# Kernel tuning notes

Hardware: AMD Instinct MI355X
Metric: run time of the kernel (lower is better)

The kernel has to match this reference:

```python
import jax, jax.numpy as jnp
import numpy as np


def _gcn_conv(X, src, dst, norm, W, n_nodes):
    # gather + normalized aggregate (SpMM) then dense linear (GEMM)
    msg = X[src] * norm[:, None]                       # [E, F]
    agg = jax.ops.segment_sum(msg, dst, num_segments=n_nodes)  # [N, F]
    return agg @ W                                     # [N, F_out]


def setup_inputs() -> dict:
    key = jax.random.key(0)
    k1, k2, k3, k4, k5 = jax.random.split(key, 5)
    N, E, D_IN, D_HID, D_OUT = 50000, 800000, 128, 128, 64
    X = jax.random.normal(k1, (N, D_IN), dtype=jnp.float32)
    edge_index = jax.random.randint(k2, (2, E), 0, N, dtype=jnp.int64)
    s = 1.0 / np.sqrt(D_IN)
    W1 = jax.random.normal(k3, (D_IN, D_HID), dtype=jnp.float32) * s
    W2 = jax.random.normal(k4, (D_HID, D_HID), dtype=jnp.float32) * s
    W3 = jax.random.normal(k5, (D_HID, D_OUT), dtype=jnp.float32) * s
    return {"X": X, "edge_index": edge_index, "W1": W1, "W2": W2, "W3": W3}


def reference(X, edge_index, W1, W2, W3):
    n_nodes = X.shape[0]
    src, dst = edge_index[0], edge_index[1]
    # symmetric degree normalization D^-1/2 A D^-1/2 (degrees from edge list)
    ones = jnp.ones(src.shape[0], dtype=X.dtype)
    deg = jax.ops.segment_sum(ones, dst, num_segments=n_nodes)
    deg = jnp.maximum(deg, 1.0)
    dinv = jax.lax.rsqrt(deg)
    norm = dinv[src] * dinv[dst]                       # [E]
    h = jax.nn.relu(_gcn_conv(X, src, dst, norm, W1, n_nodes))
    h = jax.nn.relu(_gcn_conv(h, src, dst, norm, W2, n_nodes))
    h = jax.nn.relu(_gcn_conv(h, src, dst, norm, W3, n_nodes))
    return jax.nn.softmax(h, axis=-1)
```

## Files before the change

kernel.cpp:

```cpp
#include <hip/hip_runtime.h>
#include <hip/hip_bf16.h>

typedef __attribute__((ext_vector_type(8))) short short8;
typedef __attribute__((ext_vector_type(4))) short short4v;
typedef __attribute__((ext_vector_type(4))) float f32x4;

static inline size_t ws_align(size_t x) { return (x + 511) & ~((size_t)511); }

static __device__ inline unsigned short f2bf(float f) {
    __hip_bfloat16 h = __float2bfloat16(f);
    return __builtin_bit_cast(unsigned short, h);
}

static __device__ inline float bf2f(unsigned short u) {
    unsigned int x = ((unsigned int)u) << 16;
    return __builtin_bit_cast(float, x);
}

__global__ void sniff_kernel(const unsigned short* __restrict__ w1,
                             const unsigned int* __restrict__ ei,
                             int* __restrict__ flags) {
    int i = threadIdx.x;
    unsigned e = (w1[2 * i] >> 7) & 0xFF;
    unsigned long long m1 = __ballot(e >= 100 && e <= 130);
    unsigned long long m2 = __ballot(ei[2 * i + 1] == 0u);
    if (i == 0) {
        flags[0] = (__popcll(m1) < 48) ? 1 : 0;
        flags[1] = (__popcll(m2) >= 48) ? 1 : 0;
    }
}

__global__ void hist_kernel(const int* __restrict__ ei, const int* __restrict__ flags,
                            int* __restrict__ counts, int* __restrict__ loff, int E) {
    int e = blockIdx.x * blockDim.x + threadIdx.x;
    if (e < E) {
        int d = flags[1] ? ei[2 * (size_t)E + 2 * e] : ei[(size_t)E + e];
        loff[e] = atomicAdd(&counts[d], 1);
    }
}

__global__ __launch_bounds__(256) void alloc_kernel(const int* __restrict__ counts,
                                                    float* __restrict__ dinv,
                                                    int* __restrict__ rowptr,
                                                    int* __restrict__ total, int N) {
    int n = blockIdx.x * blockDim.x + threadIdx.x;
    int lane = threadIdx.x & 63;
    int c = (n < N) ? counts[n] : 0;
    if (n < N) {
        int d = (c < 1) ? 1 : c;
        dinv[n] = rsqrtf((float)d);
    }
    int incl = c;
#pragma unroll
    for (int off = 1; off < 64; off <<= 1) {
        int v = __shfl_up(incl, off, 64);
        if (lane >= off) incl += v;
    }
    int wavetot = __shfl(incl, 63, 64);
    int base = 0;
    if (lane == 0) base = atomicAdd(total, wavetot);
    base = __shfl(base, 0, 64);
    if (n < N) rowptr[n] = base + incl - c;
}

__global__ void fill_kernel(const int* __restrict__ ei, const int* __restrict__ flags,
                            const float* __restrict__ dinv, const int* __restrict__ rowptr,
                            const int* __restrict__ loff, int2* __restrict__ edgedat, int E) {
    int e = blockIdx.x * blockDim.x + threadIdx.x;
    if (e < E) {
        int s, d;
        if (flags[1]) {
            s = ei[2 * e];
            d = ei[2 * (size_t)E + 2 * e];
        } else {
            s = ei[e];
            d = ei[(size_t)E + e];
        }
        int pos = rowptr[d] + loff[e];
        float wt = dinv[s] * dinv[d];
        edgedat[pos] = make_int2(s, __float_as_int(wt));
    }
}


template <int FOUT>
__global__ __launch_bounds__(256) void gemm_kernel(const void* __restrict__ Araw, int a_follows,
                                                   const void* __restrict__ Wraw,
                                                   const int* __restrict__ flags,
                                                   unsigned short* __restrict__ out, int Nrows) {
    constexpr int K = 128;
    constexpr int NT = FOUT / 16;
    constexpr int LDB = K + 8;
    __shared__ __align__(16) unsigned short bt[FOUT * LDB];

    const int tid = threadIdx.x;
    const int in_fp32 = flags[0];
    const int a_fp32 = a_follows & in_fp32;

    constexpr int TOT4 = K * FOUT / 4;
    if (in_fp32) {
        const float* Wf = (const float*)Wraw;
        for (int i = tid; i < TOT4; i += 256) {
            int idx = i * 4;
            int k = idx / FOUT;
            int n = idx & (FOUT - 1);
            float4 v = *(const float4*)(const void*)(Wf + idx);
            bt[(n + 0) * LDB + k] = f2bf(v.x);
            bt[(n + 1) * LDB + k] = f2bf(v.y);
            bt[(n + 2) * LDB + k] = f2bf(v.z);
            bt[(n + 3) * LDB + k] = f2bf(v.w);
        }
    } else {
        const unsigned short* Ws = (const unsigned short*)Wraw;
        for (int i = tid; i < TOT4; i += 256) {
            int idx = i * 4;
            int k = idx / FOUT;
            int n = idx & (FOUT - 1);
            short4v v = *(const short4v*)(const void*)(Ws + idx);
#pragma unroll
            for (int j = 0; j < 4; j++) bt[(n + j) * LDB + k] = ((const unsigned short*)&v)[j];
        }
    }

    const int wave = tid >> 6;
    const int lane = tid & 63;
    const int quad = lane >> 4;
    const int r16 = lane & 15;

    short8 afrag[2][4];
#pragma unroll
    for (int t = 0; t < 2; t++) {
        int arow = blockIdx.x * 128 + t * 64 + wave * 16 + r16;
        if (arow > Nrows - 1) arow = Nrows - 1;
        if (a_fp32) {
            const float* Ap = (const float*)Araw + (size_t)arow * K + quad * 8;
#pragma unroll
            for (int kk = 0; kk < 4; kk++) {
                float4 f0 = *(const float4*)(const void*)(Ap + kk * 32);
                float4 f1 = *(const float4*)(const void*)(Ap + kk * 32 + 4);
                short8 r;
                r[0] = (short)f2bf(f0.x); r[1] = (short)f2bf(f0.y);
                r[2] = (short)f2bf(f0.z); r[3] = (short)f2bf(f0.w);
                r[4] = (short)f2bf(f1.x); r[5] = (short)f2bf(f1.y);
                r[6] = (short)f2bf(f1.z); r[7] = (short)f2bf(f1.w);
                afrag[t][kk] = r;
            }
        } else {
            const unsigned short* Ap = (const unsigned short*)Araw + (size_t)arow * K + quad * 8;
#pragma unroll
            for (int kk = 0; kk < 4; kk++) afrag[t][kk] = *(const short8*)(const void*)(Ap + kk * 32);
        }
    }

    __syncthreads();

    f32x4 acc[2][NT];
#pragma unroll
    for (int t = 0; t < 2; t++)
#pragma unroll
        for (int nt = 0; nt < NT; nt++) acc[t][nt] = (f32x4){0.f, 0.f, 0.f, 0.f};

#pragma unroll
    for (int kk = 0; kk < 4; kk++) {
#pragma unroll
        for (int nt = 0; nt < NT; nt++) {
            short8 b = *(const short8*)(const void*)(&bt[(nt * 16 + r16) * LDB + kk * 32 + quad * 8]);
#pragma unroll
            for (int t = 0; t < 2; t++)
                acc[t][nt] = __builtin_amdgcn_mfma_f32_16x16x32_bf16(afrag[t][kk], b, acc[t][nt], 0, 0, 0);
        }
    }

#pragma unroll
    for (int t = 0; t < 2; t++) {
#pragma unroll
        for (int nt = 0; nt < NT; nt++) {
#pragma unroll
            for (int r = 0; r < 4; r++) {
                float v = acc[t][nt][r];
                float o = __shfl_xor(v, 1, 64);
                int row = blockIdx.x * 128 + t * 64 + wave * 16 + quad * 4 + r;
                if (((lane & 1) == 0) && row < Nrows) {
                    __hip_bfloat162 pk;
                    pk.x = __float2bfloat16(v);
                    pk.y = __float2bfloat16(o);
                    *(__hip_bfloat162*)(out + (size_t)row * FOUT + nt * 16 + r16) = pk;
                }
            }
        }
    }
}


__global__ __launch_bounds__(256) void spmm128_kernel(const int2* __restrict__ edgedat,
                                                      const int* __restrict__ rowptr,
                                                      const int* __restrict__ counts,
                                                      const unsigned short* __restrict__ Hin,
                                                      unsigned short* __restrict__ Hout, int N) {
    int wid = (blockIdx.x * 256 + threadIdx.x) >> 6;
    if (wid >= N) return;
    int lane = threadIdx.x & 63;
    int grp = lane >> 4;
    int gl = lane & 15;
    int n = __builtin_amdgcn_readfirstlane(wid);
    int start = __builtin_amdgcn_readfirstlane(rowptr[n]);
    int len = __builtin_amdgcn_readfirstlane(counts[n]);
    const int2* ep = edgedat + start;

    float acc[8];
#pragma unroll
    for (int u = 0; u < 8; u++) acc[u] = 0.f;

    int j = 0;
    for (; j + 8 <= len; j += 8) {
        int2 e0 = ep[j + grp];
        int2 e1 = ep[j + 4 + grp];
        short8 h0 = *(const short8*)(const void*)(Hin + (size_t)e0.x * 128 + gl * 8);
        short8 h1 = *(const short8*)(const void*)(Hin + (size_t)e1.x * 128 + gl * 8);
        float w0 = __int_as_float(e0.y);
        float w1 = __int_as_float(e1.y);
#pragma unroll
        for (int u = 0; u < 8; u++) acc[u] += w0 * bf2f((unsigned short)h0[u]);
#pragma unroll
        for (int u = 0; u < 8; u++) acc[u] += w1 * bf2f((unsigned short)h1[u]);
    }
    for (; j + 4 <= len; j += 4) {
        int2 e = ep[j + grp];
        short8 h = *(const short8*)(const void*)(Hin + (size_t)e.x * 128 + gl * 8);
        float w = __int_as_float(e.y);
#pragma unroll
        for (int u = 0; u < 8; u++) acc[u] += w * bf2f((unsigned short)h[u]);
    }
    int rem = len - j;
    if (grp < rem) {
        int2 e = ep[j + grp];
        short8 h = *(const short8*)(const void*)(Hin + (size_t)e.x * 128 + gl * 8);
        float w = __int_as_float(e.y);
#pragma unroll
        for (int u = 0; u < 8; u++) acc[u] += w * bf2f((unsigned short)h[u]);
    }

#pragma unroll
    for (int u = 0; u < 8; u++) {
        acc[u] += __shfl_xor(acc[u], 16, 64);
        acc[u] += __shfl_xor(acc[u], 32, 64);
    }

    if (grp == 0) {
        short8 o;
#pragma unroll
        for (int u = 0; u < 8; u++) o[u] = (short)f2bf(fmaxf(acc[u], 0.f));
        *(short8*)(void*)(Hout + (size_t)n * 128 + gl * 8) = o;
    }
}


__global__ __launch_bounds__(256) void spmm64_softmax_kernel(const int2* __restrict__ edgedat,
                                                             const int* __restrict__ rowptr,
                                                             const int* __restrict__ counts,
                                                             const unsigned short* __restrict__ Hin,
                                                             const int* __restrict__ flags,
                                                             void* __restrict__ Out, int N) {
    int wid = (blockIdx.x * 256 + threadIdx.x) >> 6;
    if (wid >= N) return;
    int lane = threadIdx.x & 63;
    int grp = lane >> 3;
    int gl = lane & 7;
    int n = __builtin_amdgcn_readfirstlane(wid);
    int start = __builtin_amdgcn_readfirstlane(rowptr[n]);
    int len = __builtin_amdgcn_readfirstlane(counts[n]);
    const int2* ep = edgedat + start;

    float acc[8];
#pragma unroll
    for (int u = 0; u < 8; u++) acc[u] = 0.f;

    int j = 0;
    for (; j + 16 <= len; j += 16) {
        int2 e0 = ep[j + grp];
        int2 e1 = ep[j + 8 + grp];
        short8 h0 = *(const short8*)(const void*)(Hin + (size_t)e0.x * 64 + gl * 8);
        short8 h1 = *(const short8*)(const void*)(Hin + (size_t)e1.x * 64 + gl * 8);
        float w0 = __int_as_float(e0.y);
        float w1 = __int_as_float(e1.y);
#pragma unroll
        for (int u = 0; u < 8; u++) acc[u] += w0 * bf2f((unsigned short)h0[u]);
#pragma unroll
        for (int u = 0; u < 8; u++) acc[u] += w1 * bf2f((unsigned short)h1[u]);
    }
    for (; j + 8 <= len; j += 8) {
        int2 e = ep[j + grp];
        short8 h = *(const short8*)(const void*)(Hin + (size_t)e.x * 64 + gl * 8);
        float w = __int_as_float(e.y);
#pragma unroll
        for (int u = 0; u < 8; u++) acc[u] += w * bf2f((unsigned short)h[u]);
    }
    int rem = len - j;
    if (grp < rem) {
        int2 e = ep[j + grp];
        short8 h = *(const short8*)(const void*)(Hin + (size_t)e.x * 64 + gl * 8);
        float w = __int_as_float(e.y);
#pragma unroll
        for (int u = 0; u < 8; u++) acc[u] += w * bf2f((unsigned short)h[u]);
    }

#pragma unroll
    for (int u = 0; u < 8; u++) {
        acc[u] += __shfl_xor(acc[u], 8, 64);
        acc[u] += __shfl_xor(acc[u], 16, 64);
        acc[u] += __shfl_xor(acc[u], 32, 64);
    }

#pragma unroll
    for (int u = 0; u < 8; u++) acc[u] = fmaxf(acc[u], 0.f);

    float m = acc[0];
#pragma unroll
    for (int u = 1; u < 8; u++) m = fmaxf(m, acc[u]);
#pragma unroll
    for (int off = 1; off < 8; off <<= 1) m = fmaxf(m, __shfl_xor(m, off, 64));

    float ex[8];
    float s = 0.f;
#pragma unroll
    for (int u = 0; u < 8; u++) {
        ex[u] = __expf(acc[u] - m);
        s += ex[u];
    }
#pragma unroll
    for (int off = 1; off < 8; off <<= 1) s += __shfl_xor(s, off, 64);
    float inv = 1.0f / s;

    if (grp == 0) {
        if (flags[0]) {
            float* op = (float*)Out + (size_t)n * 64 + gl * 8;
            float4 v0, v1;
            v0.x = ex[0] * inv; v0.y = ex[1] * inv; v0.z = ex[2] * inv; v0.w = ex[3] * inv;
            v1.x = ex[4] * inv; v1.y = ex[5] * inv; v1.z = ex[6] * inv; v1.w = ex[7] * inv;
            *(float4*)(void*)op = v0;
            *(float4*)(void*)(op + 4) = v1;
        } else {
            short8 o;
#pragma unroll
            for (int u = 0; u < 8; u++) o[u] = (short)f2bf(ex[u] * inv);
            *(short8*)(void*)((unsigned short*)Out + (size_t)n * 64 + gl * 8) = o;
        }
    }
}


extern "C" void kernel_launch(void* const* d_in, const int* in_sizes, int n_in,
                              void* d_out, int out_size, void* d_ws, size_t ws_size,
                              hipStream_t stream) {
    const void* X  = d_in[0];
    const int*  ei = (const int*)d_in[1];
    const void* W1 = d_in[2];
    const void* W2 = d_in[3];
    const void* W3 = d_in[4];

    const int N = in_sizes[0] / 128;
    const int E = in_sizes[1] / 2;

    char* ws = (char*)d_ws;
    size_t off = 0;
    int* counts = (int*)(ws + off);   off += ws_align((size_t)N * 4);
    int* total  = (int*)(ws + off);   off += ws_align(64);
    const size_t zero_bytes = off;
    int* flags    = (int*)(ws + off);   off += ws_align(64);
    int* rowptr   = (int*)(ws + off);   off += ws_align((size_t)N * 4);
    float* dinv   = (float*)(ws + off); off += ws_align((size_t)N * 4);
    int* loff     = (int*)(ws + off);   off += ws_align((size_t)E * 4);
    int2* edgedat = (int2*)(ws + off);  off += ws_align((size_t)E * 8);
    unsigned short* HA = (unsigned short*)(ws + off); off += ws_align((size_t)N * 128 * 2);
    unsigned short* HB = (unsigned short*)(ws + off); off += ws_align((size_t)N * 128 * 2);

    hipMemsetAsync(d_ws, 0, zero_bytes, stream);

    sniff_kernel<<<1, 64, 0, stream>>>((const unsigned short*)W1, (const unsigned int*)ei, flags);
    hist_kernel<<<(E + 255) / 256, 256, 0, stream>>>(ei, flags, counts, loff, E);
    alloc_kernel<<<(N + 255) / 256, 256, 0, stream>>>(counts, dinv, rowptr, total, N);
    fill_kernel<<<(E + 255) / 256, 256, 0, stream>>>(ei, flags, dinv, rowptr, loff, edgedat, E);

    const int gblocks = (N + 127) / 128;
    const int sblocks = (N * 64 + 255) / 256;

    gemm_kernel<128><<<gblocks, 256, 0, stream>>>(X, 1, W1, flags, HA, N);
    spmm128_kernel<<<sblocks, 256, 0, stream>>>(edgedat, rowptr, counts, HA, HB, N);
    gemm_kernel<128><<<gblocks, 256, 0, stream>>>(HB, 0, W2, flags, HA, N);
    spmm128_kernel<<<sblocks, 256, 0, stream>>>(edgedat, rowptr, counts, HA, HB, N);
    gemm_kernel<64><<<gblocks, 256, 0, stream>>>(HB, 0, W3, flags, HA, N);
    spmm64_softmax_kernel<<<sblocks, 256, 0, stream>>>(edgedat, rowptr, counts, HA, flags, d_out, N);
}
```

Measured before the change: 273.9 us.

## Fuse first GEMM with degree histogram and dtype sniff into one launch

```diff
diff --git a/kernel.cpp b/kernel.cpp
--- a/kernel.cpp
+++ b/kernel.cpp
@@ -17,27 +17,161 @@
     return __builtin_bit_cast(float, x);
 }
 
-__global__ void sniff_kernel(const unsigned short* __restrict__ w1,
-                             const unsigned int* __restrict__ ei,
-                             int* __restrict__ flags) {
-    int i = threadIdx.x;
-    unsigned e = (w1[2 * i] >> 7) & 0xFF;
-    unsigned long long m1 = __ballot(e >= 100 && e <= 130);
-    unsigned long long m2 = __ballot(ei[2 * i + 1] == 0u);
-    if (i == 0) {
-        flags[0] = (__popcll(m1) < 48) ? 1 : 0;
-        flags[1] = (__popcll(m2) >= 48) ? 1 : 0;
-    }
-}
-
-__global__ void hist_kernel(const int* __restrict__ ei, const int* __restrict__ flags,
-                            int* __restrict__ counts, int* __restrict__ loff, int E) {
-    int e = blockIdx.x * blockDim.x + threadIdx.x;
-    if (e < E) {
-        int d = flags[1] ? ei[2 * (size_t)E + 2 * e] : ei[(size_t)E + e];
-        loff[e] = atomicAdd(&counts[d], 1);
-    }
-}
+
+template <int FOUT>
+static __device__ inline void gemm64_body(const void* __restrict__ Araw, int a_fp32,
+                                          const void* __restrict__ Wraw, int w_fp32,
+                                          unsigned short* __restrict__ out,
+                                          int N, int blk) {
+    constexpr int K = 128;
+    constexpr int NT = FOUT / 16;
+    constexpr int LDB = K + 8;
+    constexpr int LDA = K + 8;
+    __shared__ __align__(16) unsigned short bt[FOUT * LDB];
+    __shared__ __align__(16) unsigned short atile[64 * LDA];
+
+    const int tid = threadIdx.x;
+    const int base = blk * 64;
+
+    constexpr int TOT4 = K * FOUT / 4;
+    if (w_fp32) {
+        const float* Wf = (const float*)Wraw;
+        for (int i = tid; i < TOT4; i += 256) {
+            int idx = i * 4;
+            int k = idx / FOUT;
+            int n = idx & (FOUT - 1);
+            float4 v = *(const float4*)(const void*)(Wf + idx);
+            bt[(n + 0) * LDB + k] = f2bf(v.x);
+            bt[(n + 1) * LDB + k] = f2bf(v.y);
+            bt[(n + 2) * LDB + k] = f2bf(v.z);
+            bt[(n + 3) * LDB + k] = f2bf(v.w);
+        }
+    } else {
+        const unsigned short* Ws = (const unsigned short*)Wraw;
+        for (int i = tid; i < TOT4; i += 256) {
+            int idx = i * 4;
+            int k = idx / FOUT;
+            int n = idx & (FOUT - 1);
+            short4v v = *(const short4v*)(const void*)(Ws + idx);
+#pragma unroll
+            for (int j = 0; j < 4; j++) bt[(n + j) * LDB + k] = ((const unsigned short*)&v)[j];
+        }
+    }
+
+    if (a_fp32) {
+        const float* Af = (const float*)Araw;
+#pragma unroll
+        for (int i = 0; i < 8; i++) {
+            int e4 = i * 256 + tid;
+            int elem = e4 * 4;
+            int r = elem >> 7;
+            int c = elem & 127;
+            int srow = base + r;
+            if (srow > N - 1) srow = N - 1;
+            float4 v = *(const float4*)(const void*)(Af + (size_t)srow * K + c);
+            unsigned short* dst = &atile[r * LDA + c];
+            dst[0] = f2bf(v.x); dst[1] = f2bf(v.y); dst[2] = f2bf(v.z); dst[3] = f2bf(v.w);
+        }
+    } else {
+        const unsigned short* Ab = (const unsigned short*)Araw;
+#pragma unroll
+        for (int i = 0; i < 4; i++) {
+            int e8 = i * 256 + tid;
+            int elem = e8 * 8;
+            int r = elem >> 7;
+            int c = elem & 127;
+            int srow = base + r;
+            if (srow > N - 1) srow = N - 1;
+            *(short8*)(void*)(&atile[r * LDA + c]) =
+                *(const short8*)(const void*)(Ab + (size_t)srow * K + c);
+        }
+    }
+
+    __syncthreads();
+
+    const int wave = tid >> 6;
+    const int lane = tid & 63;
+    const int quad = lane >> 4;
+    const int r16 = lane & 15;
+
+    short8 afrag[4];
+#pragma unroll
+    for (int kk = 0; kk < 4; kk++)
+        afrag[kk] = *(const short8*)(const void*)(&atile[(wave * 16 + r16) * LDA + kk * 32 + quad * 8]);
+
+    f32x4 acc[NT];
+#pragma unroll
+    for (int nt = 0; nt < NT; nt++) acc[nt] = (f32x4){0.f, 0.f, 0.f, 0.f};
+
+#pragma unroll
+    for (int kk = 0; kk < 4; kk++) {
+#pragma unroll
+        for (int nt = 0; nt < NT; nt++) {
+            short8 b = *(const short8*)(const void*)(&bt[(nt * 16 + r16) * LDB + kk * 32 + quad * 8]);
+            acc[nt] = __builtin_amdgcn_mfma_f32_16x16x32_bf16(afrag[kk], b, acc[nt], 0, 0, 0);
+        }
+    }
+
+#pragma unroll
+    for (int nt = 0; nt < NT; nt++) {
+#pragma unroll
+        for (int r = 0; r < 4; r++) {
+            float v = acc[nt][r];
+            float o = __shfl_xor(v, 1, 64);
+            int row = base + wave * 16 + quad * 4 + r;
+            if (((lane & 1) == 0) && row < N) {
+                __hip_bfloat162 pk;
+                pk.x = __float2bfloat16(v);
+                pk.y = __float2bfloat16(o);
+                *(__hip_bfloat162*)(out + (size_t)row * FOUT + nt * 16 + r16) = pk;
+            }
+        }
+    }
+}
+
+
+__global__ __launch_bounds__(256) void gemm1_hist_kernel(const void* __restrict__ Xraw,
+                                                         const unsigned short* __restrict__ w1s,
+                                                         const int* __restrict__ ei,
+                                                         int* __restrict__ counts,
+                                                         int* __restrict__ loff,
+                                                         int* __restrict__ flags,
+                                                         unsigned short* __restrict__ out,
+                                                         int N, int E, int gblocks) {
+    const int tid = threadIdx.x;
+    const int lane = tid & 63;
+
+    unsigned ew = (w1s[2 * lane] >> 7) & 0xFF;
+    unsigned long long m1 = __ballot(ew >= 100 && ew <= 130);
+    const int in_fp32 = (__popcll(m1) < 48) ? 1 : 0;
+
+    if (blockIdx.x >= gblocks) {
+        unsigned long long m2 = __ballot(((const unsigned int*)ei)[2 * lane + 1] == 0u);
+        const int ei64 = (__popcll(m2) >= 48) ? 1 : 0;
+        if (blockIdx.x == gblocks && tid == 0) {
+            flags[0] = in_fp32;
+            flags[1] = ei64;
+        }
+        int e = (blockIdx.x - gblocks) * 256 + tid;
+        if (e < E) {
+            int d = ei64 ? ei[2 * (size_t)E + 2 * e] : ei[(size_t)E + e];
+            loff[e] = atomicAdd(&counts[d], 1);
+        }
+        return;
+    }
+
+    gemm64_body<128>(Xraw, in_fp32, (const void*)w1s, in_fp32, out, N, blockIdx.x);
+}
+
+
+template <int FOUT>
+__global__ __launch_bounds__(256) void gemm_kernel(const void* __restrict__ Araw,
+                                                   const void* __restrict__ Wraw,
+                                                   const int* __restrict__ flags,
+                                                   unsigned short* __restrict__ out, int N) {
+    gemm64_body<FOUT>(Araw, 0, Wraw, flags[0], out, N, blockIdx.x);
+}
+
 
 __global__ __launch_bounds__(256) void alloc_kernel(const int* __restrict__ counts,
                                                     float* __restrict__ dinv,
@@ -79,115 +213,6 @@
         int pos = rowptr[d] + loff[e];
         float wt = dinv[s] * dinv[d];
         edgedat[pos] = make_int2(s, __float_as_int(wt));
-    }
-}
-
-
-template <int FOUT>
-__global__ __launch_bounds__(256) void gemm_kernel(const void* __restrict__ Araw, int a_follows,
-                                                   const void* __restrict__ Wraw,
-                                                   const int* __restrict__ flags,
-                                                   unsigned short* __restrict__ out, int Nrows) {
-    constexpr int K = 128;
-    constexpr int NT = FOUT / 16;
-    constexpr int LDB = K + 8;
-    __shared__ __align__(16) unsigned short bt[FOUT * LDB];
-
-    const int tid = threadIdx.x;
-    const int in_fp32 = flags[0];
-    const int a_fp32 = a_follows & in_fp32;
-
-    constexpr int TOT4 = K * FOUT / 4;
-    if (in_fp32) {
-        const float* Wf = (const float*)Wraw;
-        for (int i = tid; i < TOT4; i += 256) {
-            int idx = i * 4;
-            int k = idx / FOUT;
-            int n = idx & (FOUT - 1);
-            float4 v = *(const float4*)(const void*)(Wf + idx);
-            bt[(n + 0) * LDB + k] = f2bf(v.x);
-            bt[(n + 1) * LDB + k] = f2bf(v.y);
-            bt[(n + 2) * LDB + k] = f2bf(v.z);
-            bt[(n + 3) * LDB + k] = f2bf(v.w);
-        }
-    } else {
-        const unsigned short* Ws = (const unsigned short*)Wraw;
-        for (int i = tid; i < TOT4; i += 256) {
-            int idx = i * 4;
-            int k = idx / FOUT;
-            int n = idx & (FOUT - 1);
-            short4v v = *(const short4v*)(const void*)(Ws + idx);
-#pragma unroll
-            for (int j = 0; j < 4; j++) bt[(n + j) * LDB + k] = ((const unsigned short*)&v)[j];
-        }
-    }
-
-    const int wave = tid >> 6;
-    const int lane = tid & 63;
-    const int quad = lane >> 4;
-    const int r16 = lane & 15;
-
-    short8 afrag[2][4];
-#pragma unroll
-    for (int t = 0; t < 2; t++) {
-        int arow = blockIdx.x * 128 + t * 64 + wave * 16 + r16;
-        if (arow > Nrows - 1) arow = Nrows - 1;
-        if (a_fp32) {
-            const float* Ap = (const float*)Araw + (size_t)arow * K + quad * 8;
-#pragma unroll
-            for (int kk = 0; kk < 4; kk++) {
-                float4 f0 = *(const float4*)(const void*)(Ap + kk * 32);
-                float4 f1 = *(const float4*)(const void*)(Ap + kk * 32 + 4);
-                short8 r;
-                r[0] = (short)f2bf(f0.x); r[1] = (short)f2bf(f0.y);
-                r[2] = (short)f2bf(f0.z); r[3] = (short)f2bf(f0.w);
-                r[4] = (short)f2bf(f1.x); r[5] = (short)f2bf(f1.y);
-                r[6] = (short)f2bf(f1.z); r[7] = (short)f2bf(f1.w);
-                afrag[t][kk] = r;
-            }
-        } else {
-            const unsigned short* Ap = (const unsigned short*)Araw + (size_t)arow * K + quad * 8;
-#pragma unroll
-            for (int kk = 0; kk < 4; kk++) afrag[t][kk] = *(const short8*)(const void*)(Ap + kk * 32);
-        }
-    }
-
-    __syncthreads();
-
-    f32x4 acc[2][NT];
-#pragma unroll
-    for (int t = 0; t < 2; t++)
-#pragma unroll
-        for (int nt = 0; nt < NT; nt++) acc[t][nt] = (f32x4){0.f, 0.f, 0.f, 0.f};
-
-#pragma unroll
-    for (int kk = 0; kk < 4; kk++) {
-#pragma unroll
-        for (int nt = 0; nt < NT; nt++) {
-            short8 b = *(const short8*)(const void*)(&bt[(nt * 16 + r16) * LDB + kk * 32 + quad * 8]);
-#pragma unroll
-            for (int t = 0; t < 2; t++)
-                acc[t][nt] = __builtin_amdgcn_mfma_f32_16x16x32_bf16(afrag[t][kk], b, acc[t][nt], 0, 0, 0);
-        }
-    }
-
-#pragma unroll
-    for (int t = 0; t < 2; t++) {
-#pragma unroll
-        for (int nt = 0; nt < NT; nt++) {
-#pragma unroll
-            for (int r = 0; r < 4; r++) {
-                float v = acc[t][nt][r];
-                float o = __shfl_xor(v, 1, 64);
-                int row = blockIdx.x * 128 + t * 64 + wave * 16 + quad * 4 + r;
-                if (((lane & 1) == 0) && row < Nrows) {
-                    __hip_bfloat162 pk;
-                    pk.x = __float2bfloat16(v);
-                    pk.y = __float2bfloat16(o);
-                    *(__hip_bfloat162*)(out + (size_t)row * FOUT + nt * 16 + r16) = pk;
-                }
-            }
-        }
     }
 }
 
@@ -376,18 +401,18 @@
 
     hipMemsetAsync(d_ws, 0, zero_bytes, stream);
 
-    sniff_kernel<<<1, 64, 0, stream>>>((const unsigned short*)W1, (const unsigned int*)ei, flags);
-    hist_kernel<<<(E + 255) / 256, 256, 0, stream>>>(ei, flags, counts, loff, E);
+    const int gblocks = (N + 63) / 64;
+    const int hblocks = (E + 255) / 256;
+    const int sblocks = (N * 64 + 255) / 256;
+
+    gemm1_hist_kernel<<<gblocks + hblocks, 256, 0, stream>>>(
+        X, (const unsigned short*)W1, ei, counts, loff, flags, HA, N, E, gblocks);
     alloc_kernel<<<(N + 255) / 256, 256, 0, stream>>>(counts, dinv, rowptr, total, N);
-    fill_kernel<<<(E + 255) / 256, 256, 0, stream>>>(ei, flags, dinv, rowptr, loff, edgedat, E);
-
-    const int gblocks = (N + 127) / 128;
-    const int sblocks = (N * 64 + 255) / 256;
-
-    gemm_kernel<128><<<gblocks, 256, 0, stream>>>(X, 1, W1, flags, HA, N);
+    fill_kernel<<<hblocks, 256, 0, stream>>>(ei, flags, dinv, rowptr, loff, edgedat, E);
+
     spmm128_kernel<<<sblocks, 256, 0, stream>>>(edgedat, rowptr, counts, HA, HB, N);
-    gemm_kernel<128><<<gblocks, 256, 0, stream>>>(HB, 0, W2, flags, HA, N);
+    gemm_kernel<128><<<gblocks, 256, 0, stream>>>(HB, W2, flags, HA, N);
     spmm128_kernel<<<sblocks, 256, 0, stream>>>(edgedat, rowptr, counts, HA, HB, N);
-    gemm_kernel<64><<<gblocks, 256, 0, stream>>>(HB, 0, W3, flags, HA, N);
+    gemm_kernel<64><<<gblocks, 256, 0, stream>>>(HB, W3, flags, HA, N);
     spmm64_softmax_kernel<<<sblocks, 256, 0, stream>>>(edgedat, rowptr, counts, HA, flags, d_out, N);
 }
```

Result: no change. 276.5 us (+0.9%).
